# Performance work log

Measured on AMD Instinct MI355X. Metric: run time of the kernel, lower is better.

Reference implementation:

```python
import jax, jax.numpy as jnp
import numpy as np

ALPHA = 0.12
BETA = 0.88
OMEGA = 6.0
PHI_BASE = 0.0
B, T, D = 4, 4096, 2048


def setup_inputs() -> dict:
    key = jax.random.key(0)
    k1, = jax.random.split(key, 1)
    x = jax.random.normal(k1, (B, T, D), dtype=jnp.float32)
    gate = jnp.asarray(-2.0, dtype=jnp.float32)          # nn.Parameter gate_init
    input_scale = jnp.asarray(4.0, dtype=jnp.float32)     # nn.Parameter init 4.0
    mem_state = jnp.zeros((1, 1, D), dtype=jnp.float32)   # persistent buffer
    return {"x": x, "gate": gate, "input_scale": input_scale,
            "mem_state": mem_state, "step_idx": 0}


def reference(x, gate, input_scale, mem_state, step_idx):
    Bn, Tn, Dn = x.shape
    dtype = x.dtype
    # EMA recurrence: m_t = beta * m_{t-1} + alpha * input_scale * x_t
    u = (ALPHA * input_scale) * x                         # [B,T,D]
    m0 = jnp.broadcast_to(mem_state[:, 0, :], (Bn, Dn))   # [B,D]

    def step(m, u_t):
        m = BETA * m + u_t
        return m, m

    _, ms = jax.lax.scan(step, m0, jnp.swapaxes(u, 0, 1))  # [T,B,D]
    ms = jnp.swapaxes(ms, 0, 1)                            # [B,T,D]

    # log-periodic phase rotation per step (scalar angle per t)
    t_glob = jnp.arange(1, Tn + 1, dtype=dtype) + jnp.asarray(step_idx, dtype)
    theta = (OMEGA * jnp.log1p(t_glob) + PHI_BASE) % (2.0 * jnp.pi)  # [T]
    c = jnp.cos(theta)[None, :, None]
    s = jnp.sin(theta)[None, :, None]
    half = Dn // 2  # D even -> no tail
    a = ms[..., :half]
    b = ms[..., half:2 * half]
    m_rot = jnp.concatenate([a * c - b * s, a * s + b * c], axis=-1)  # [B,T,D]

    # residual gated output: y = x + sigmoid(gate) * m_seq
    return x + jax.nn.sigmoid(gate) * m_rot
```

## Files before the change

### kernel.cpp

```cpp
#include <hip/hip_runtime.h>
#include <math.h>

#define ALPHA 0.12f
#define BETA  0.88f
#define OMEGA 6.0f
#define TWO_PI 6.28318530717958647692f

constexpr int Bn   = 4;
constexpr int Tn   = 4096;
constexpr int Dn   = 2048;
constexpr int HALF = Dn / 2;
constexpr int L    = 64;
constexpr int NC   = Tn / L;

constexpr float beta_pow(int n) {
    float r = 1.0f;
    for (int i = 0; i < n; ++i) r *= BETA;
    return r;
}
constexpr float BETA_L = beta_pow(L);

__global__ void k_theta(float* __restrict__ ctab, float* __restrict__ stab,
                        const int* __restrict__ step_idx) {
    int t = blockIdx.x * blockDim.x + threadIdx.x;
    if (t >= Tn) return;
    float tg = (float)(t + 1 + *step_idx);
    float theta = fmodf(OMEGA * log1pf(tg), TWO_PI);
    ctab[t] = cosf(theta);
    stab[t] = sinf(theta);
}

__global__ void k_chunksum(const float* __restrict__ x,
                           const float* __restrict__ input_scale,
                           float* __restrict__ S) {
    int gid = blockIdx.x * blockDim.x + threadIdx.x;
    int d = gid & (Dn - 1);
    int c = (gid >> 11) & (NC - 1);
    int b = gid >> 17;
    const float sc = ALPHA * (*input_scale);
    const float* xp = x + ((size_t)b * Tn + (size_t)c * L) * Dn + d;
    float m = 0.0f;
#pragma unroll 8
    for (int i = 0; i < L; ++i) {
        m = BETA * m + sc * xp[(size_t)i * Dn];
    }
    S[gid] = m;
}

__global__ void k_carry(float* __restrict__ SC,
                        const float* __restrict__ mem_state) {
    int gid = blockIdx.x * blockDim.x + threadIdx.x;
    int d = gid & (Dn - 1);
    int b = gid >> 11;
    float m = mem_state[d];
    for (int c = 0; c < NC; ++c) {
        size_t idx = ((size_t)(b * NC + c) * Dn) + d;
        float s = SC[idx];
        SC[idx] = m;
        m = BETA_L * m + s;
    }
}

__global__ void k_final(const float* __restrict__ x,
                        const float* __restrict__ gate,
                        const float* __restrict__ input_scale,
                        const float* __restrict__ ctab,
                        const float* __restrict__ stab,
                        const float* __restrict__ C,
                        float* __restrict__ out) {
    int gid = blockIdx.x * blockDim.x + threadIdx.x;
    int p = gid & (HALF - 1);
    int c = (gid >> 10) & (NC - 1);
    int b = gid >> 16;

    const float sc  = ALPHA * (*input_scale);
    const float sig = 1.0f / (1.0f + expf(-(*gate)));

    size_t base = ((size_t)b * Tn + (size_t)c * L) * Dn;
    const float* xa = x + base + p;
    const float* xb = x + base + p + HALF;
    float* oa = out + base + p;
    float* ob = out + base + p + HALF;

    size_t cbase = (size_t)(b * NC + c) * Dn;
    float ma = C[cbase + p];
    float mb = C[cbase + p + HALF];

    int t0 = c * L;
#pragma unroll 4
    for (int i = 0; i < L; ++i) {
        float va = xa[(size_t)i * Dn];
        float vb = xb[(size_t)i * Dn];
        ma = BETA * ma + sc * va;
        mb = BETA * mb + sc * vb;
        float cth = ctab[t0 + i];
        float sth = stab[t0 + i];
        oa[(size_t)i * Dn] = va + sig * (ma * cth - mb * sth);
        ob[(size_t)i * Dn] = vb + sig * (ma * sth + mb * cth);
    }
}

extern "C" void kernel_launch(void* const* d_in, const int* in_sizes, int n_in,
                              void* d_out, int out_size, void* d_ws, size_t ws_size,
                              hipStream_t stream) {
    const float* x           = (const float*)d_in[0];
    const float* gate        = (const float*)d_in[1];
    const float* input_scale = (const float*)d_in[2];
    const float* mem_state   = (const float*)d_in[3];
    const int*   step_idx    = (const int*)d_in[4];
    float* out = (float*)d_out;

    float* ws   = (float*)d_ws;
    float* ctab = ws;
    float* stab = ws + Tn;
    float* SC   = ws + 2 * Tn;

    k_theta<<<Tn / 256, 256, 0, stream>>>(ctab, stab, step_idx);
    k_chunksum<<<(Bn * NC * Dn) / 256, 256, 0, stream>>>(x, input_scale, SC);
    k_carry<<<(Bn * Dn) / 256, 256, 0, stream>>>(SC, mem_state);
    k_final<<<(Bn * NC * HALF) / 256, 256, 0, stream>>>(x, gate, input_scale,
                                                        ctab, stab, SC, out);
}
```

Measured before the change: 275.4 us.

## Vectorize scan kernels to float4, merge theta and carry kernels, nontemporal stores

Result: faster. 259.4 us (-5.8%).

```diff
diff --git a/kernel.cpp b/kernel.cpp
--- a/kernel.cpp
+++ b/kernel.cpp
@@ -13,6 +13,8 @@
 constexpr int L    = 64;
 constexpr int NC   = Tn / L;
 
+typedef float fx4 __attribute__((ext_vector_type(4)));
+
 constexpr float beta_pow(int n) {
     float r = 1.0f;
     for (int i = 0; i < n; ++i) r *= BETA;
@@ -20,44 +22,47 @@
 }
 constexpr float BETA_L = beta_pow(L);
 
-__global__ void k_theta(float* __restrict__ ctab, float* __restrict__ stab,
-                        const int* __restrict__ step_idx) {
-    int t = blockIdx.x * blockDim.x + threadIdx.x;
-    if (t >= Tn) return;
-    float tg = (float)(t + 1 + *step_idx);
-    float theta = fmodf(OMEGA * log1pf(tg), TWO_PI);
-    ctab[t] = cosf(theta);
-    stab[t] = sinf(theta);
-}
-
 __global__ void k_chunksum(const float* __restrict__ x,
                            const float* __restrict__ input_scale,
                            float* __restrict__ S) {
     int gid = blockIdx.x * blockDim.x + threadIdx.x;
-    int d = gid & (Dn - 1);
-    int c = (gid >> 11) & (NC - 1);
-    int b = gid >> 17;
+    int d4 = gid & (Dn / 4 - 1);
+    int c  = (gid >> 9) & (NC - 1);
+    int b  = gid >> 15;
     const float sc = ALPHA * (*input_scale);
-    const float* xp = x + ((size_t)b * Tn + (size_t)c * L) * Dn + d;
-    float m = 0.0f;
+
+    const fx4* xp = (const fx4*)(x + ((size_t)b * Tn + (size_t)c * L) * Dn) + d4;
+    fx4 m = (fx4)(0.0f);
 #pragma unroll 8
     for (int i = 0; i < L; ++i) {
-        m = BETA * m + sc * xp[(size_t)i * Dn];
+        fx4 v = xp[(size_t)i * (Dn / 4)];
+        m = BETA * m + sc * v;
     }
-    S[gid] = m;
+    ((fx4*)S)[gid] = m;
 }
 
-__global__ void k_carry(float* __restrict__ SC,
-                        const float* __restrict__ mem_state) {
-    int gid = blockIdx.x * blockDim.x + threadIdx.x;
-    int d = gid & (Dn - 1);
-    int b = gid >> 11;
-    float m = mem_state[d];
-    for (int c = 0; c < NC; ++c) {
-        size_t idx = ((size_t)(b * NC + c) * Dn) + d;
-        float s = SC[idx];
-        SC[idx] = m;
-        m = BETA_L * m + s;
+__global__ void k_mid(float* __restrict__ SC,
+                      const float* __restrict__ mem_state,
+                      float* __restrict__ ctab, float* __restrict__ stab,
+                      const int* __restrict__ step_idx) {
+    if (blockIdx.x < 8) {
+        int gid = blockIdx.x * blockDim.x + threadIdx.x;
+        int d4 = gid & (Dn / 4 - 1);
+        int b  = gid >> 9;
+        fx4 m = ((const fx4*)mem_state)[d4];
+        fx4* scp = (fx4*)SC;
+        for (int c = 0; c < NC; ++c) {
+            int idx = (b * NC + c) * (Dn / 4) + d4;
+            fx4 s = scp[idx];
+            scp[idx] = m;
+            m = BETA_L * m + s;
+        }
+    } else {
+        int t = (blockIdx.x - 8) * blockDim.x + threadIdx.x;
+        float tg = (float)(t + 1 + *step_idx);
+        float theta = fmodf(OMEGA * log1pf(tg), TWO_PI);
+        ctab[t] = cosf(theta);
+        stab[t] = sinf(theta);
     }
 }
 
@@ -69,34 +74,36 @@
                         const float* __restrict__ C,
                         float* __restrict__ out) {
     int gid = blockIdx.x * blockDim.x + threadIdx.x;
-    int p = gid & (HALF - 1);
-    int c = (gid >> 10) & (NC - 1);
-    int b = gid >> 16;
+    int p4 = gid & (HALF / 4 - 1);
+    int c  = (gid >> 8) & (NC - 1);
+    int b  = gid >> 14;
 
     const float sc  = ALPHA * (*input_scale);
     const float sig = 1.0f / (1.0f + expf(-(*gate)));
 
     size_t base = ((size_t)b * Tn + (size_t)c * L) * Dn;
-    const float* xa = x + base + p;
-    const float* xb = x + base + p + HALF;
-    float* oa = out + base + p;
-    float* ob = out + base + p + HALF;
+    const fx4* xa = (const fx4*)(x + base) + p4;
+    const fx4* xb = (const fx4*)(x + base + HALF) + p4;
+    fx4* oa = (fx4*)(out + base) + p4;
+    fx4* ob = (fx4*)(out + base + HALF) + p4;
 
     size_t cbase = (size_t)(b * NC + c) * Dn;
-    float ma = C[cbase + p];
-    float mb = C[cbase + p + HALF];
+    fx4 ma = ((const fx4*)(C + cbase))[p4];
+    fx4 mb = ((const fx4*)(C + cbase + HALF))[p4];
 
     int t0 = c * L;
 #pragma unroll 4
     for (int i = 0; i < L; ++i) {
-        float va = xa[(size_t)i * Dn];
-        float vb = xb[(size_t)i * Dn];
+        fx4 va = xa[(size_t)i * (Dn / 4)];
+        fx4 vb = xb[(size_t)i * (Dn / 4)];
         ma = BETA * ma + sc * va;
         mb = BETA * mb + sc * vb;
         float cth = ctab[t0 + i];
         float sth = stab[t0 + i];
-        oa[(size_t)i * Dn] = va + sig * (ma * cth - mb * sth);
-        ob[(size_t)i * Dn] = vb + sig * (ma * sth + mb * cth);
+        fx4 ra = va + sig * (ma * cth - mb * sth);
+        fx4 rb = vb + sig * (ma * sth + mb * cth);
+        __builtin_nontemporal_store(ra, &oa[(size_t)i * (Dn / 4)]);
+        __builtin_nontemporal_store(rb, &ob[(size_t)i * (Dn / 4)]);
     }
 }
 
@@ -115,9 +122,8 @@
     float* stab = ws + Tn;
     float* SC   = ws + 2 * Tn;
 
-    k_theta<<<Tn / 256, 256, 0, stream>>>(ctab, stab, step_idx);
-    k_chunksum<<<(Bn * NC * Dn) / 256, 256, 0, stream>>>(x, input_scale, SC);
-    k_carry<<<(Bn * Dn) / 256, 256, 0, stream>>>(SC, mem_state);
-    k_final<<<(Bn * NC * HALF) / 256, 256, 0, stream>>>(x, gate, input_scale,
-                                                        ctab, stab, SC, out);
+    k_chunksum<<<(Bn * NC * Dn / 4) / 256, 256, 0, stream>>>(x, input_scale, SC);
+    k_mid<<<8 + Tn / 256, 256, 0, stream>>>(SC, mem_state, ctab, stab, step_idx);
+    k_final<<<(Bn * NC * HALF / 4) / 256, 256, 0, stream>>>(x, gate, input_scale,
+                                                            ctab, stab, SC, out);
 }
```
